# Optimization experiments

Measured on AMD Instinct MI355X. Metric: run time of the kernel, lower is better.

## Reference

```python
import jax, jax.numpy as jnp
import numpy as np

SIZE = (128.0, 128.0, 128.0)
FEATURE_BLOCK_IDS = (1, 2, 3)


def _trilerp(feat, coords, power):
    # feat: [B, D, H, W, C]; coords: [B, N, 3] in [0, 1]
    B = coords.shape[0]
    scale = jnp.asarray([0.5 ** power * SIZE[0],
                         0.5 ** power * SIZE[1],
                         0.5 ** power * SIZE[2]], dtype=coords.dtype)
    hi = float(min(feat.shape[1:4])) - 1.01
    idx = jnp.clip(coords * scale, 0.01, hi)  # [B, N, 3]
    ix, iy, iz = idx[..., 0], idx[..., 1], idx[..., 2]
    x1, x2 = jnp.floor(ix), jnp.ceil(ix)
    y1, y2 = jnp.floor(iy), jnp.ceil(iy)
    z1, z2 = jnp.floor(iz), jnp.ceil(iz)
    b = jnp.arange(B)[:, None]  # broadcast batch index

    def g(xi, yi, zi):
        return feat[b, xi.astype(jnp.int32), yi.astype(jnp.int32), zi.astype(jnp.int32)]

    wx, wx2 = (ix - x1)[..., None], (x2 - ix)[..., None]
    wy, wy2 = (iy - y1)[..., None], (y2 - iy)[..., None]
    wz, wz2 = (iz - z1)[..., None], (z2 - iz)[..., None]

    # z = z1 plane
    lerp_x1 = g(x2, y1, z1) * wx + g(x1, y1, z1) * wx2
    lerp_x2 = g(x2, y2, z1) * wx + g(x1, y2, z1) * wx2
    lerp_y1 = lerp_x2 * wy + lerp_x1 * wy2
    # z = z2 plane
    lerp_x1 = g(x2, y1, z2) * wx + g(x1, y1, z2) * wx2
    lerp_x2 = g(x2, y2, z2) * wx + g(x1, y2, z2) * wx2
    lerp_y2 = lerp_x2 * wy + lerp_x1 * wy2
    return lerp_y2 * wz + lerp_y1 * wz2  # [B, N, C]


def setup_inputs() -> dict:
    key = jax.random.key(0)
    ks = jax.random.split(key, 7)
    B, N = 2, 50000
    return {
        'features0': jax.random.normal(ks[0], (B, 128, 128, 128, 1), jnp.float32),
        'features1': jax.random.normal(ks[1], (B, 64, 64, 64, 32), jnp.float32),
        'features2': jax.random.normal(ks[2], (B, 32, 32, 32, 64), jnp.float32),
        'features3': jax.random.normal(ks[3], (B, 16, 16, 16, 128), jnp.float32),
        'features4': jax.random.normal(ks[4], (B, 8, 8, 8, 256), jnp.float32),
        'mesh_coords': jax.random.uniform(ks[5], (B, N, 3), jnp.float32),
        'mesh_features': jax.random.normal(ks[6], (B, N, 3), jnp.float32),
    }


def reference(features0, features1, features2, features3, features4, mesh_coords, mesh_features):
    feats = [features0, features1, features2, features3, features4]
    # mesh_coords is [B, N, 3] -> one coord group, reshape is identity
    sampled = [_trilerp(feats[i], mesh_coords, i) for i in FEATURE_BLOCK_IDS]
    out = jnp.concatenate(sampled, axis=-1)
    return jnp.concatenate([out, mesh_features], axis=-1)
```

## Files before the change

kernel.cpp:

```cpp
#include <hip/hip_runtime.h>


typedef float floatx4 __attribute__((ext_vector_type(4)));

#define G 4
#define THREADS 256

__global__ __launch_bounds__(THREADS, 8) void trilerp_fused_kernel(
    const float* __restrict__ f1,
    const float* __restrict__ f2,
    const float* __restrict__ f3,
    const float* __restrict__ coords,
    const float* __restrict__ meshf,
    float* __restrict__ out,
    int N, int P)
{
    __shared__ float rowbuf[G * 227];
    const int tid = (int)threadIdx.x;
    const int p0  = (int)blockIdx.x * G;

    if (tid < G * 56) {
        const int pt   = tid / 56;
        const int role = tid - pt * 56;
        const int p    = p0 + pt;
        if (p < P) {
            const int lvl = (role < 8) ? 0 : ((role < 24) ? 1 : 2);
            const int D   = 64 >> lvl;
            const int C   = 32 << lvl;
            const int c4  = role - ((lvl == 0) ? 0 : ((lvl == 1) ? 8 : 24));
            const int ocb = (lvl == 0) ? 0 : ((lvl == 1) ? 32 : 96);
            const float* fb = (lvl == 0) ? f1 : ((lvl == 1) ? f2 : f3);

            const int b = (p >= N) ? 1 : 0;

            const float cx = coords[p * 3 + 0];
            const float cy = coords[p * 3 + 1];
            const float cz = coords[p * 3 + 2];

            const float scale = (float)D;
            const float hi    = (float)((double)D - 1.01);

            const float ix = fminf(fmaxf(cx * scale, 0.01f), hi);
            const float iy = fminf(fmaxf(cy * scale, 0.01f), hi);
            const float iz = fminf(fmaxf(cz * scale, 0.01f), hi);

            const float x1f = floorf(ix), x2f = ceilf(ix);
            const float y1f = floorf(iy), y2f = ceilf(iy);
            const float z1f = floorf(iz), z2f = ceilf(iz);
            const int x1 = (int)x1f, x2 = (int)x2f;
            const int y1 = (int)y1f, y2 = (int)y2f;
            const int z1 = (int)z1f, z2 = (int)z2f;

            const float wx = ix - x1f, wx2 = x2f - ix;
            const float wy = iy - y1f, wy2 = y2f - iy;
            const float wz = iz - z1f, wz2 = z2f - iz;

            #define OFF(X, Y, Z) ((((((b) * D + (X)) * D + (Y)) * D + (Z)) * C) + c4 * 4)
            const floatx4 v111 = *(const floatx4*)(fb + OFF(x1, y1, z1));
            const floatx4 v211 = *(const floatx4*)(fb + OFF(x2, y1, z1));
            const floatx4 v121 = *(const floatx4*)(fb + OFF(x1, y2, z1));
            const floatx4 v221 = *(const floatx4*)(fb + OFF(x2, y2, z1));
            const floatx4 v112 = *(const floatx4*)(fb + OFF(x1, y1, z2));
            const floatx4 v212 = *(const floatx4*)(fb + OFF(x2, y1, z2));
            const floatx4 v122 = *(const floatx4*)(fb + OFF(x1, y2, z2));
            const floatx4 v222 = *(const floatx4*)(fb + OFF(x2, y2, z2));
            #undef OFF

            const floatx4 lx1a = v211 * wx + v111 * wx2;
            const floatx4 lx2a = v221 * wx + v121 * wx2;
            const floatx4 ly1v = lx2a * wy + lx1a * wy2;
            const floatx4 lx1b = v212 * wx + v112 * wx2;
            const floatx4 lx2b = v222 * wx + v122 * wx2;
            const floatx4 ly2v = lx2b * wy + lx1b * wy2;
            const floatx4 r    = ly2v * wz + ly1v * wz2;

            float* rb = rowbuf + pt * 227 + ocb + c4 * 4;
            rb[0] = r.x; rb[1] = r.y; rb[2] = r.z; rb[3] = r.w;
        }
    } else if (tid < G * 56 + G * 3) {
        const int i  = tid - G * 56;
        const int pt = i / 3, c = i - pt * 3;
        const int p  = p0 + pt;
        if (p < P) rowbuf[pt * 227 + 224 + c] = meshf[p * 3 + c];
    }

    __syncthreads();

    const int nrow = min(G, P - p0);
    if (nrow == G) {
        if (tid < 227) {
            const floatx4 v = *(const floatx4*)(rowbuf + tid * 4);
            __builtin_nontemporal_store(v, (floatx4*)(out + (size_t)p0 * 227) + tid);
        }
    } else if (nrow > 0) {
        for (int i = tid; i < nrow * 227; i += THREADS)
            out[(size_t)p0 * 227 + i] = rowbuf[i];
    }
}

extern "C" void kernel_launch(void* const* d_in, const int* in_sizes, int n_in,
                              void* d_out, int out_size, void* d_ws, size_t ws_size,
                              hipStream_t stream) {
    const float* f1     = (const float*)d_in[1];
    const float* f2     = (const float*)d_in[2];
    const float* f3     = (const float*)d_in[3];
    const float* coords = (const float*)d_in[5];
    const float* meshf  = (const float*)d_in[6];
    float* out = (float*)d_out;

    const int B = in_sizes[1] / (64 * 64 * 64 * 32);
    const int N = in_sizes[5] / (B * 3);
    const int P = B * N;

    const int grid = (P + G - 1) / G;
    trilerp_fused_kernel<<<dim3(grid), dim3(THREADS), 0, stream>>>(
        f1, f2, f3, coords, meshf, out, N, P);
}
```

Measured before the change: 214.6 us.

## Bucket-sort points by spatial cell before trilinear gather for cache locality

Adds a histogram, scan and scatter pass that bins points into a 16^3 grid per batch, then runs the gather kernel over points in sorted order. Blocks are also remapped so contiguous segments go to the same XCD. Spatially nearby points then reuse the same feature-grid cache lines in L2 and MALL. The cost is three extra kernel launches, a memset, a single-block scan, and scattered output rows, since each row is written to its original position.

```diff
diff --git a/kernel.cpp b/kernel.cpp
--- a/kernel.cpp
+++ b/kernel.cpp
@@ -2,28 +2,107 @@
 
 
 typedef float floatx4 __attribute__((ext_vector_type(4)));
-
+typedef float f4u __attribute__((ext_vector_type(4), aligned(4)));
+
+#define NBINS 8192
 #define G 4
 #define THREADS 256
 
-__global__ __launch_bounds__(THREADS, 8) void trilerp_fused_kernel(
-    const float* __restrict__ f1,
-    const float* __restrict__ f2,
+__device__ __forceinline__ int point_batch(int p, int N) {
+    int b = 0;
+    while (p >= N) { p -= N; ++b; }
+    return b;
+}
+
+__device__ __forceinline__ int bucket_of(const float* __restrict__ coords,
+                                         int p, int N) {
+    const float cx = coords[p * 3 + 0];
+    const float cy = coords[p * 3 + 1];
+    const float cz = coords[p * 3 + 2];
+    int bx = (int)(cx * 16.0f); bx = bx < 0 ? 0 : (bx > 15 ? 15 : bx);
+    int by = (int)(cy * 16.0f); by = by < 0 ? 0 : (by > 15 ? 15 : by);
+    int bz = (int)(cz * 16.0f); bz = bz < 0 ? 0 : (bz > 15 ? 15 : bz);
+    return ((point_batch(p, N) * 16 + bx) * 16 + by) * 16 + bz;
+}
+
+__global__ __launch_bounds__(256) void hist_kernel(
+    const float* __restrict__ coords, unsigned* __restrict__ bins,
+    int N, int P)
+{
+    const int p = blockIdx.x * 256 + (int)threadIdx.x;
+    if (p < P) atomicAdd(&bins[bucket_of(coords, p, N)], 1u);
+}
+
+__global__ __launch_bounds__(1024) void scan_kernel(unsigned* __restrict__ bins)
+{
+    __shared__ unsigned part[1024];
+    const int t = threadIdx.x;
+    unsigned loc[8];
+    unsigned s = 0;
+    for (int i = 0; i < 8; ++i) {
+        unsigned v = bins[t * 8 + i];
+        loc[i] = s;
+        s += v;
+    }
+    part[t] = s;
+    __syncthreads();
+    for (int off = 1; off < 1024; off <<= 1) {
+        unsigned v = (t >= off) ? part[t - off] : 0u;
+        __syncthreads();
+        part[t] += v;
+        __syncthreads();
+    }
+    const unsigned base = (t == 0) ? 0u : part[t - 1];
+    for (int i = 0; i < 8; ++i) bins[t * 8 + i] = base + loc[i];
+}
+
+__global__ __launch_bounds__(256) void scatter_kernel(
+    const float* __restrict__ coords, const float* __restrict__ meshf,
+    unsigned* __restrict__ bins, unsigned* __restrict__ perm,
+    float* __restrict__ csort, float* __restrict__ msort,
+    int N, int P)
+{
+    const int p = blockIdx.x * 256 + (int)threadIdx.x;
+    if (p < P) {
+        const unsigned pos = atomicAdd(&bins[bucket_of(coords, p, N)], 1u);
+        perm[pos] = (unsigned)p;
+        csort[pos * 3 + 0] = coords[p * 3 + 0];
+        csort[pos * 3 + 1] = coords[p * 3 + 1];
+        csort[pos * 3 + 2] = coords[p * 3 + 2];
+        msort[pos * 3 + 0] = meshf[p * 3 + 0];
+        msort[pos * 3 + 1] = meshf[p * 3 + 1];
+        msort[pos * 3 + 2] = meshf[p * 3 + 2];
+    }
+}
+
+__device__ __forceinline__ int seg_swz(int lo, int S) {
+    const int q = S >> 3, r = S & 7;
+    const int xcd = lo & 7, j = lo >> 3;
+    return (xcd < r ? xcd * (q + 1) : r * (q + 1) + (xcd - r) * q) + j;
+}
+
+template<int SORTED>
+__device__ __forceinline__ void fused_body(
+    const float* __restrict__ f1, const float* __restrict__ f2,
     const float* __restrict__ f3,
-    const float* __restrict__ coords,
-    const float* __restrict__ meshf,
-    float* __restrict__ out,
-    int N, int P)
+    const float* __restrict__ cin,
+    const float* __restrict__ min_,
+    const unsigned* __restrict__ perm,
+    float* __restrict__ out, int blk, int N, int P)
 {
     __shared__ float rowbuf[G * 227];
+    __shared__ int   rowp[G];
     const int tid = (int)threadIdx.x;
-    const int p0  = (int)blockIdx.x * G;
+    const int s0  = blk * G;
 
     if (tid < G * 56) {
         const int pt   = tid / 56;
         const int role = tid - pt * 56;
-        const int p    = p0 + pt;
-        if (p < P) {
+        const int slot = s0 + pt;
+        if (slot < P) {
+            const int p = SORTED ? (int)perm[slot] : slot;
+            if (role == 0) rowp[pt] = p;
+
             const int lvl = (role < 8) ? 0 : ((role < 24) ? 1 : 2);
             const int D   = 64 >> lvl;
             const int C   = 32 << lvl;
@@ -33,9 +112,9 @@
 
             const int b = (p >= N) ? 1 : 0;
 
-            const float cx = coords[p * 3 + 0];
-            const float cy = coords[p * 3 + 1];
-            const float cz = coords[p * 3 + 2];
+            const float cx = cin[slot * 3 + 0];
+            const float cy = cin[slot * 3 + 1];
+            const float cz = cin[slot * 3 + 2];
 
             const float scale = (float)D;
             const float hi    = (float)((double)D - 1.01);
@@ -80,22 +159,52 @@
     } else if (tid < G * 56 + G * 3) {
         const int i  = tid - G * 56;
         const int pt = i / 3, c = i - pt * 3;
-        const int p  = p0 + pt;
-        if (p < P) rowbuf[pt * 227 + 224 + c] = meshf[p * 3 + c];
+        const int slot = s0 + pt;
+        if (slot < P) rowbuf[pt * 227 + 224 + c] = min_[slot * 3 + c];
     }
 
     __syncthreads();
 
-    const int nrow = min(G, P - p0);
-    if (nrow == G) {
-        if (tid < 227) {
-            const floatx4 v = *(const floatx4*)(rowbuf + tid * 4);
-            __builtin_nontemporal_store(v, (floatx4*)(out + (size_t)p0 * 227) + tid);
+    if (tid < G * 57) {
+        const int pt = tid / 57;
+        const int j  = tid - pt * 57;
+        const int slot = s0 + pt;
+        if (slot < P) {
+            const int p = SORTED ? rowp[pt] : slot;
+            const float* rb = rowbuf + pt * 227;
+            float* o = out + (size_t)p * 227;
+            if (j < 56) {
+                floatx4 v;
+                v.x = rb[j * 4 + 0]; v.y = rb[j * 4 + 1];
+                v.z = rb[j * 4 + 2]; v.w = rb[j * 4 + 3];
+                __builtin_nontemporal_store(v, (f4u*)(o + j * 4));
+            } else {
+                __builtin_nontemporal_store(rb[224], o + 224);
+                __builtin_nontemporal_store(rb[225], o + 225);
+                __builtin_nontemporal_store(rb[226], o + 226);
+            }
         }
-    } else if (nrow > 0) {
-        for (int i = tid; i < nrow * 227; i += THREADS)
-            out[(size_t)p0 * 227 + i] = rowbuf[i];
-    }
+    }
+}
+
+__global__ __launch_bounds__(THREADS, 8) void trilerp_sorted_kernel(
+    const float* __restrict__ f1, const float* __restrict__ f2,
+    const float* __restrict__ f3, const float* __restrict__ csort,
+    const float* __restrict__ msort, const unsigned* __restrict__ perm,
+    float* __restrict__ out, int N, int P, int nblk)
+{
+    const int blk = seg_swz((int)blockIdx.x, nblk);
+    fused_body<1>(f1, f2, f3, csort, msort, perm, out, blk, N, P);
+}
+
+__global__ __launch_bounds__(THREADS, 8) void trilerp_fused_kernel(
+    const float* __restrict__ f1, const float* __restrict__ f2,
+    const float* __restrict__ f3, const float* __restrict__ coords,
+    const float* __restrict__ meshf, float* __restrict__ out,
+    int N, int P)
+{
+    fused_body<0>(f1, f2, f3, coords, meshf, nullptr, out,
+                  (int)blockIdx.x, N, P);
 }
 
 extern "C" void kernel_launch(void* const* d_in, const int* in_sizes, int n_in,
@@ -112,7 +221,27 @@
     const int N = in_sizes[5] / (B * 3);
     const int P = B * N;
 
-    const int grid = (P + G - 1) / G;
-    trilerp_fused_kernel<<<dim3(grid), dim3(THREADS), 0, stream>>>(
-        f1, f2, f3, coords, meshf, out, N, P);
-}
+    const size_t ws_need = (size_t)NBINS * 4 + (size_t)P * 4
+                         + (size_t)P * 12 + (size_t)P * 12;
+    unsigned* bins  = (unsigned*)d_ws;
+    unsigned* perm  = bins + NBINS;
+    float*    csort = (float*)(perm + P);
+    float*    msort = csort + (size_t)P * 3;
+    const bool do_sort = (d_ws != nullptr) && (ws_size >= ws_need);
+
+    const int nblk = (P + G - 1) / G;
+
+    if (do_sort) {
+        hipMemsetAsync(bins, 0, NBINS * 4, stream);
+        const int nbp = (P + 255) / 256;
+        hist_kernel<<<dim3(nbp), dim3(256), 0, stream>>>(coords, bins, N, P);
+        scan_kernel<<<dim3(1), dim3(1024), 0, stream>>>(bins);
+        scatter_kernel<<<dim3(nbp), dim3(256), 0, stream>>>(
+            coords, meshf, bins, perm, csort, msort, N, P);
+        trilerp_sorted_kernel<<<dim3(nblk), dim3(THREADS), 0, stream>>>(
+            f1, f2, f3, csort, msort, perm, out, N, P, nblk);
+    } else {
+        trilerp_fused_kernel<<<dim3(nblk), dim3(THREADS), 0, stream>>>(
+            f1, f2, f3, coords, meshf, out, N, P);
+    }
+}
```

Result: slower. 233.3 us (+8.7%).

## Convert trilerp kernel to persistent grid-stride blocks with double-buffered row staging

Applied to the files above, without the earlier changes.

Replaces the one-block-per-4-points launch with a fixed grid of 2048 persistent blocks that loop over point groups. Per-thread role setup (level, channel offset, scale) is hoisted out of the loop, and the shared row buffer is double-buffered so the next iteration's writes don't race the current store phase. This aims to cut block launch and scheduling overhead across the many small blocks, at the cost of fewer blocks in flight to hide gather latency and a loop with a barrier per iteration.

```diff
diff --git a/kernel.cpp b/kernel.cpp
--- a/kernel.cpp
+++ b/kernel.cpp
@@ -5,96 +5,106 @@
 
 #define G 4
 #define THREADS 256
+#define PBLOCKS 2048
 
-__global__ __launch_bounds__(THREADS, 8) void trilerp_fused_kernel(
+__global__ __launch_bounds__(THREADS, 8) void trilerp_persist_kernel(
     const float* __restrict__ f1,
     const float* __restrict__ f2,
     const float* __restrict__ f3,
     const float* __restrict__ coords,
     const float* __restrict__ meshf,
     float* __restrict__ out,
-    int N, int P)
+    int N, int P, int nblk)
 {
-    __shared__ float rowbuf[G * 227];
+    __shared__ float rowbuf[2][G * 227];
     const int tid = (int)threadIdx.x;
-    const int p0  = (int)blockIdx.x * G;
 
-    if (tid < G * 56) {
-        const int pt   = tid / 56;
-        const int role = tid - pt * 56;
-        const int p    = p0 + pt;
-        if (p < P) {
-            const int lvl = (role < 8) ? 0 : ((role < 24) ? 1 : 2);
-            const int D   = 64 >> lvl;
-            const int C   = 32 << lvl;
-            const int c4  = role - ((lvl == 0) ? 0 : ((lvl == 1) ? 8 : 24));
-            const int ocb = (lvl == 0) ? 0 : ((lvl == 1) ? 32 : 96);
-            const float* fb = (lvl == 0) ? f1 : ((lvl == 1) ? f2 : f3);
+    const int  pt        = tid / 56;
+    const int  role      = tid - pt * 56;
+    const bool is_gather = tid < G * 56;
+    const bool is_mesh   = (tid >= G * 56) && (tid < G * 56 + G * 3);
+    const int  mi        = tid - G * 56;
+    const int  mpt       = mi / 3;
+    const int  mc        = mi - mpt * 3;
 
-            const int b = (p >= N) ? 1 : 0;
+    const int lvl = (role < 8) ? 0 : ((role < 24) ? 1 : 2);
+    const int D   = 64 >> lvl;
+    const int C   = 32 << lvl;
+    const int c4  = role - ((lvl == 0) ? 0 : ((lvl == 1) ? 8 : 24));
+    const int ocb = (lvl == 0) ? 0 : ((lvl == 1) ? 32 : 96);
+    const float* fb = (lvl == 0) ? f1 : ((lvl == 1) ? f2 : f3);
+    const float scale = (float)D;
+    const float hi    = (float)((double)D - 1.01);
 
-            const float cx = coords[p * 3 + 0];
-            const float cy = coords[p * 3 + 1];
-            const float cz = coords[p * 3 + 2];
+    int par = 0;
+    for (int blk = (int)blockIdx.x; blk < nblk; blk += PBLOCKS, par ^= 1) {
+        const int p0 = blk * G;
+        float* rbw = rowbuf[par];
 
-            const float scale = (float)D;
-            const float hi    = (float)((double)D - 1.01);
+        if (is_gather) {
+            const int p = p0 + pt;
+            if (p < P) {
+                const int b = (p >= N) ? 1 : 0;
 
-            const float ix = fminf(fmaxf(cx * scale, 0.01f), hi);
-            const float iy = fminf(fmaxf(cy * scale, 0.01f), hi);
-            const float iz = fminf(fmaxf(cz * scale, 0.01f), hi);
+                const float cx = coords[p * 3 + 0];
+                const float cy = coords[p * 3 + 1];
+                const float cz = coords[p * 3 + 2];
 
-            const float x1f = floorf(ix), x2f = ceilf(ix);
-            const float y1f = floorf(iy), y2f = ceilf(iy);
-            const float z1f = floorf(iz), z2f = ceilf(iz);
-            const int x1 = (int)x1f, x2 = (int)x2f;
-            const int y1 = (int)y1f, y2 = (int)y2f;
-            const int z1 = (int)z1f, z2 = (int)z2f;
+                const float ix = fminf(fmaxf(cx * scale, 0.01f), hi);
+                const float iy = fminf(fmaxf(cy * scale, 0.01f), hi);
+                const float iz = fminf(fmaxf(cz * scale, 0.01f), hi);
 
-            const float wx = ix - x1f, wx2 = x2f - ix;
-            const float wy = iy - y1f, wy2 = y2f - iy;
-            const float wz = iz - z1f, wz2 = z2f - iz;
+                const float x1f = floorf(ix), x2f = ceilf(ix);
+                const float y1f = floorf(iy), y2f = ceilf(iy);
+                const float z1f = floorf(iz), z2f = ceilf(iz);
+                const int x1 = (int)x1f, x2 = (int)x2f;
+                const int y1 = (int)y1f, y2 = (int)y2f;
+                const int z1 = (int)z1f, z2 = (int)z2f;
 
-            #define OFF(X, Y, Z) ((((((b) * D + (X)) * D + (Y)) * D + (Z)) * C) + c4 * 4)
-            const floatx4 v111 = *(const floatx4*)(fb + OFF(x1, y1, z1));
-            const floatx4 v211 = *(const floatx4*)(fb + OFF(x2, y1, z1));
-            const floatx4 v121 = *(const floatx4*)(fb + OFF(x1, y2, z1));
-            const floatx4 v221 = *(const floatx4*)(fb + OFF(x2, y2, z1));
-            const floatx4 v112 = *(const floatx4*)(fb + OFF(x1, y1, z2));
-            const floatx4 v212 = *(const floatx4*)(fb + OFF(x2, y1, z2));
-            const floatx4 v122 = *(const floatx4*)(fb + OFF(x1, y2, z2));
-            const floatx4 v222 = *(const floatx4*)(fb + OFF(x2, y2, z2));
-            #undef OFF
+                const float wx = ix - x1f, wx2 = x2f - ix;
+                const float wy = iy - y1f, wy2 = y2f - iy;
+                const float wz = iz - z1f, wz2 = z2f - iz;
 
-            const floatx4 lx1a = v211 * wx + v111 * wx2;
-            const floatx4 lx2a = v221 * wx + v121 * wx2;
-            const floatx4 ly1v = lx2a * wy + lx1a * wy2;
-            const floatx4 lx1b = v212 * wx + v112 * wx2;
-            const floatx4 lx2b = v222 * wx + v122 * wx2;
-            const floatx4 ly2v = lx2b * wy + lx1b * wy2;
-            const floatx4 r    = ly2v * wz + ly1v * wz2;
+                #define OFF(X, Y, Z) ((((((b) * D + (X)) * D + (Y)) * D + (Z)) * C) + c4 * 4)
+                const floatx4 v111 = *(const floatx4*)(fb + OFF(x1, y1, z1));
+                const floatx4 v211 = *(const floatx4*)(fb + OFF(x2, y1, z1));
+                const floatx4 v121 = *(const floatx4*)(fb + OFF(x1, y2, z1));
+                const floatx4 v221 = *(const floatx4*)(fb + OFF(x2, y2, z1));
+                const floatx4 v112 = *(const floatx4*)(fb + OFF(x1, y1, z2));
+                const floatx4 v212 = *(const floatx4*)(fb + OFF(x2, y1, z2));
+                const floatx4 v122 = *(const floatx4*)(fb + OFF(x1, y2, z2));
+                const floatx4 v222 = *(const floatx4*)(fb + OFF(x2, y2, z2));
+                #undef OFF
 
-            float* rb = rowbuf + pt * 227 + ocb + c4 * 4;
-            rb[0] = r.x; rb[1] = r.y; rb[2] = r.z; rb[3] = r.w;
+                const floatx4 lx1a = v211 * wx + v111 * wx2;
+                const floatx4 lx2a = v221 * wx + v121 * wx2;
+                const floatx4 ly1v = lx2a * wy + lx1a * wy2;
+                const floatx4 lx1b = v212 * wx + v112 * wx2;
+                const floatx4 lx2b = v222 * wx + v122 * wx2;
+                const floatx4 ly2v = lx2b * wy + lx1b * wy2;
+                const floatx4 r    = ly2v * wz + ly1v * wz2;
+
+                float* rb = rbw + pt * 227 + ocb + c4 * 4;
+                rb[0] = r.x; rb[1] = r.y; rb[2] = r.z; rb[3] = r.w;
+            }
+        } else if (is_mesh) {
+            const int p = p0 + mpt;
+            if (p < P) rbw[mpt * 227 + 224 + mc] = meshf[p * 3 + mc];
         }
-    } else if (tid < G * 56 + G * 3) {
-        const int i  = tid - G * 56;
-        const int pt = i / 3, c = i - pt * 3;
-        const int p  = p0 + pt;
-        if (p < P) rowbuf[pt * 227 + 224 + c] = meshf[p * 3 + c];
-    }
 
-    __syncthreads();
+        __syncthreads();
 
-    const int nrow = min(G, P - p0);
-    if (nrow == G) {
-        if (tid < 227) {
-            const floatx4 v = *(const floatx4*)(rowbuf + tid * 4);
-            __builtin_nontemporal_store(v, (floatx4*)(out + (size_t)p0 * 227) + tid);
+        const int nrow = min(G, P - p0);
+        if (nrow == G) {
+            if (tid < 227) {
+                const floatx4 v = *(const floatx4*)(rbw + tid * 4);
+                __builtin_nontemporal_store(
+                    v, (floatx4*)(out + (size_t)p0 * 227) + tid);
+            }
+        } else if (nrow > 0) {
+            for (int i = tid; i < nrow * 227; i += THREADS)
+                out[(size_t)p0 * 227 + i] = rbw[i];
         }
-    } else if (nrow > 0) {
-        for (int i = tid; i < nrow * 227; i += THREADS)
-            out[(size_t)p0 * 227 + i] = rowbuf[i];
     }
 }
 
@@ -112,7 +122,9 @@
     const int N = in_sizes[5] / (B * 3);
     const int P = B * N;
 
-    const int grid = (P + G - 1) / G;
-    trilerp_fused_kernel<<<dim3(grid), dim3(THREADS), 0, stream>>>(
-        f1, f2, f3, coords, meshf, out, N, P);
+    const int nblk = (P + G - 1) / G;
+    const int grid = (nblk < PBLOCKS) ? nblk : PBLOCKS;
+
+    trilerp_persist_kernel<<<dim3(grid), dim3(THREADS), 0, stream>>>(
+        f1, f2, f3, coords, meshf, out, N, P, nblk);
 }
```

Result: slower. 220.6 us (+2.8%).
